# Kernel tuning notes

Hardware: AMD Instinct MI355X
Metric: run time of the kernel (lower is better)

The kernel has to match this reference:

```python
import jax, jax.numpy as jnp
import numpy as np

D_MODEL = 1024
N_HEADS = 16
D_K = D_MODEL // N_HEADS
BATCH = 2
SEQ = 2048


def setup_inputs() -> dict:
    key = jax.random.key(0)
    ks = jax.random.split(key, 6)
    scale = 1.0 / np.sqrt(D_MODEL)
    x = jax.random.normal(ks[0], (BATCH, SEQ, D_MODEL), dtype=jnp.float32)
    position_bias = jax.random.normal(ks[1], (N_HEADS, SEQ, SEQ), dtype=jnp.float32)
    w_q = jax.random.normal(ks[2], (D_MODEL, D_MODEL), dtype=jnp.float32) * scale
    w_k = jax.random.normal(ks[3], (D_MODEL, D_MODEL), dtype=jnp.float32) * scale
    w_v = jax.random.normal(ks[4], (D_MODEL, D_MODEL), dtype=jnp.float32) * scale
    w_o = jax.random.normal(ks[5], (D_MODEL, D_MODEL), dtype=jnp.float32) * scale
    return {"x": x, "position_bias": position_bias, "w_q": w_q, "w_k": w_k, "w_v": w_v, "w_o": w_o}


def reference(x, position_bias, w_q, w_k, w_v, w_o):
    B, n, _ = x.shape
    # Linear(d,d,bias=False): y = x @ W^T
    def split_heads(t):
        return t.reshape(B, n, N_HEADS, D_K).transpose(0, 2, 1, 3)  # [B,H,n,d_k]
    Q = split_heads(x @ w_q.T)
    K = split_heads(x @ w_k.T)
    V = split_heads(x @ w_v.T)
    # T5-style: no 1/sqrt(d_k) scaling
    scores = jnp.einsum('bhqd,bhkd->bhqk', Q, K) + position_bias[None]
    attn = jax.nn.softmax(scores.astype(jnp.float32), axis=-1).astype(scores.dtype)
    ctx = jnp.einsum('bhqk,bhkd->bhqd', attn, V)  # [B,H,n,d_k]
    attention = ctx.transpose(0, 2, 1, 3).reshape(B, n, D_MODEL)
    return attention @ w_o.T
```

## Files before the change

kernel.cpp:

```cpp
#include <hip/hip_runtime.h>


typedef _Float16 f16_t;
typedef _Float16 f16x8 __attribute__((ext_vector_type(8)));
typedef _Float16 f16x4 __attribute__((ext_vector_type(4)));
typedef float   floatx4 __attribute__((ext_vector_type(4)));

#define MFMA16(a, b, c)    __builtin_amdgcn_mfma_f32_16x16x32_f16((a), (b), (c), 0, 0, 0)
#define MFMA16K16(a, b, c) __builtin_amdgcn_mfma_f32_16x16x16f16((a), (b), (c), 0, 0, 0)

__global__ __launch_bounds__(256) void cvt_f32_f16(const float* __restrict__ src,
                                                   f16_t* __restrict__ dst, int n) {
  int i = (blockIdx.x * 256 + threadIdx.x) * 4;
  if (i < n) {
    floatx4 v = *(const floatx4*)(src + i);
    f16x4 o;
    o.x = (_Float16)v.x; o.y = (_Float16)v.y; o.z = (_Float16)v.z; o.w = (_Float16)v.w;
    *(f16x4*)(dst + i) = o;
  }
}

__global__ __launch_bounds__(256) void qkv_gemm(
    const f16_t* __restrict__ xb,
    const f16_t* __restrict__ wqb, const f16_t* __restrict__ wkb,
    const f16_t* __restrict__ wvb,
    f16_t* __restrict__ qb, f16_t* __restrict__ kb, f16_t* __restrict__ vb) {
  __shared__ f16_t As[128][72];
  __shared__ f16_t Bs[128][72];
  const int t = threadIdx.x;
  const int w = t >> 6, lane = t & 63, quad = lane >> 4, col = lane & 15;
  const int wm = w & 1, wn = w >> 1;
  const int mbase = blockIdx.x * 128;
  const int which = blockIdx.y >> 3;
  const int ncol0 = (blockIdx.y & 7) * 128;
  const f16_t* wsel = (which == 0) ? wqb : (which == 1) ? wkb : wvb;
  f16_t* osel = (which == 0) ? qb : (which == 1) ? kb : vb;

  floatx4 zero4 = {0.f, 0.f, 0.f, 0.f};
  floatx4 acc[4][4];
#pragma unroll
  for (int i = 0; i < 4; ++i)
#pragma unroll
    for (int j = 0; j < 4; ++j) acc[i][j] = zero4;

  for (int kt = 0; kt < 16; ++kt) {
    const int k0 = kt * 64;
#pragma unroll
    for (int rep = 0; rep < 4; ++rep) {
      int cid = t + rep * 256;
      int r = cid >> 3, c = (cid & 7) * 8;
      *(f16x8*)&As[r][c] = *(const f16x8*)(xb + (size_t)(mbase + r) * 1024 + k0 + c);
      *(f16x8*)&Bs[r][c] = *(const f16x8*)(wsel + (size_t)(ncol0 + r) * 1024 + k0 + c);
    }
    __syncthreads();
#pragma unroll
    for (int ch = 0; ch < 2; ++ch) {
      f16x8 a[4], b[4];
#pragma unroll
      for (int i = 0; i < 4; ++i)
        a[i] = *(const f16x8*)&As[wm * 64 + i * 16 + col][ch * 32 + quad * 8];
#pragma unroll
      for (int j = 0; j < 4; ++j)
        b[j] = *(const f16x8*)&Bs[wn * 64 + j * 16 + col][ch * 32 + quad * 8];
#pragma unroll
      for (int i = 0; i < 4; ++i)
#pragma unroll
        for (int j = 0; j < 4; ++j)
          acc[i][j] = MFMA16(a[i], b[j], acc[i][j]);
    }
    __syncthreads();
  }
#pragma unroll
  for (int i = 0; i < 4; ++i)
#pragma unroll
    for (int j = 0; j < 4; ++j)
#pragma unroll
      for (int rr = 0; rr < 4; ++rr) {
        int m = mbase + wm * 64 + i * 16 + quad * 4 + rr;
        int nf = ncol0 + wn * 64 + j * 16 + col;
        int h = nf >> 6, d = nf & 63;
        int bb2 = m >> 11, s = m & 2047;
        osel[(size_t)(((bb2 * 16 + h) * 2048) + s) * 64 + d] = (f16_t)acc[i][j][rr];
      }
}

__global__ __launch_bounds__(256) void out_gemm(
    const f16_t* __restrict__ ab, const f16_t* __restrict__ wob,
    float* __restrict__ outp) {
  __shared__ f16_t As[128][72];
  __shared__ f16_t Bs[128][72];
  const int t = threadIdx.x;
  const int w = t >> 6, lane = t & 63, quad = lane >> 4, col = lane & 15;
  const int wm = w & 1, wn = w >> 1;
  const int mbase = blockIdx.x * 128;
  const int nbase = blockIdx.y * 128;

  floatx4 zero4 = {0.f, 0.f, 0.f, 0.f};
  floatx4 acc[4][4];
#pragma unroll
  for (int i = 0; i < 4; ++i)
#pragma unroll
    for (int j = 0; j < 4; ++j) acc[i][j] = zero4;

  for (int kt = 0; kt < 16; ++kt) {
    const int k0 = kt * 64;
#pragma unroll
    for (int rep = 0; rep < 4; ++rep) {
      int cid = t + rep * 256;
      int r = cid >> 3, c = (cid & 7) * 8;
      *(f16x8*)&As[r][c] = *(const f16x8*)(ab + (size_t)(mbase + r) * 1024 + k0 + c);
      *(f16x8*)&Bs[r][c] = *(const f16x8*)(wob + (size_t)(nbase + r) * 1024 + k0 + c);
    }
    __syncthreads();
#pragma unroll
    for (int ch = 0; ch < 2; ++ch) {
      f16x8 a[4], b[4];
#pragma unroll
      for (int i = 0; i < 4; ++i)
        a[i] = *(const f16x8*)&As[wm * 64 + i * 16 + col][ch * 32 + quad * 8];
#pragma unroll
      for (int j = 0; j < 4; ++j)
        b[j] = *(const f16x8*)&Bs[wn * 64 + j * 16 + col][ch * 32 + quad * 8];
#pragma unroll
      for (int i = 0; i < 4; ++i)
#pragma unroll
        for (int j = 0; j < 4; ++j)
          acc[i][j] = MFMA16(a[i], b[j], acc[i][j]);
    }
    __syncthreads();
  }
#pragma unroll
  for (int i = 0; i < 4; ++i)
#pragma unroll
    for (int j = 0; j < 4; ++j)
#pragma unroll
      for (int rr = 0; rr < 4; ++rr) {
        int m = mbase + wm * 64 + i * 16 + quad * 4 + rr;
        int n = nbase + wn * 64 + j * 16 + col;
        outp[(size_t)m * 1024 + n] = acc[i][j][rr];
      }
}

__global__ __launch_bounds__(512) void attn_kernel(
    const f16_t* __restrict__ qb, const f16_t* __restrict__ kb,
    const f16_t* __restrict__ vb, const float* __restrict__ bias,
    f16_t* __restrict__ ctxb) {
  __shared__ f16_t Ks[2][64][72];
  __shared__ f16_t Vt[2][64][76];
  __shared__ f16_t biasS[64][72];

  const int t = threadIdx.x;
  const int w = t >> 6, lane = t & 63, quad = lane >> 4, col = lane & 15;
  const int bb = w >> 2, w4 = w & 3;
  const int h = blockIdx.y;
  const int qbase = blockIdx.x * 64;

  f16x8 qf[2];
  {
    const f16_t* qp = qb + (size_t)(((bb * 16 + h) * 2048) + qbase + w4 * 16 + col) * 64;
    qf[0] = *(const f16x8*)(qp + quad * 8);
    qf[1] = *(const f16x8*)(qp + 32 + quad * 8);
  }

  float mprev = -3e38f, lrun = 0.f;
  floatx4 zero4 = {0.f, 0.f, 0.f, 0.f};
  floatx4 oacc[4];
  oacc[0] = oacc[1] = oacc[2] = oacc[3] = zero4;

  for (int kt = 0; kt < 32; ++kt) {
    const int kbase = kt * 64;
#pragma unroll
    for (int rep = 0; rep < 2; ++rep) {
      int cid = t + rep * 512;
      int b2 = cid >> 9, rem = cid & 511;
      int r = rem >> 3, c = (rem & 7) * 8;
      *(f16x8*)&Ks[b2][r][c] =
          *(const f16x8*)(kb + (size_t)(((b2 * 16 + h) * 2048) + kbase + r) * 64 + c);
    }
    if (t < 256) {
      int b2 = t >> 7, rem = t & 127;
      int kk0 = (rem & 15) * 4, d0 = (rem >> 4) * 8;
      f16x8 rows[4];
#pragma unroll
      for (int j = 0; j < 4; ++j)
        rows[j] = *(const f16x8*)(vb +
            (size_t)(((b2 * 16 + h) * 2048) + kbase + kk0 + j) * 64 + d0);
#pragma unroll
      for (int d = 0; d < 8; ++d) {
        f16x4 pk;
        pk.x = rows[0][d]; pk.y = rows[1][d]; pk.z = rows[2][d]; pk.w = rows[3][d];
        *(f16x4*)&Vt[b2][d0 + d][kk0] = pk;
      }
    }
    {
      int r = t >> 3, c0 = (t & 7) * 8;
      const float* bp = bias + ((size_t)h * 2048 + qbase + r) * 2048 + kbase + c0;
      floatx4 v0 = *(const floatx4*)bp;
      floatx4 v1 = *(const floatx4*)(bp + 4);
      f16x8 bo;
      bo[0] = (_Float16)v0.x; bo[1] = (_Float16)v0.y;
      bo[2] = (_Float16)v0.z; bo[3] = (_Float16)v0.w;
      bo[4] = (_Float16)v1.x; bo[5] = (_Float16)v1.y;
      bo[6] = (_Float16)v1.z; bo[7] = (_Float16)v1.w;
      *(f16x8*)&biasS[r][c0] = bo;
    }
    __syncthreads();

    floatx4 sacc[4];
    sacc[0] = sacc[1] = sacc[2] = sacc[3] = zero4;
#pragma unroll
    for (int ch = 0; ch < 2; ++ch) {
#pragma unroll
      for (int cb = 0; cb < 4; ++cb) {
        f16x8 kf = *(const f16x8*)&Ks[bb][cb * 16 + col][ch * 32 + quad * 8];
        sacc[cb] = MFMA16(kf, qf[ch], sacc[cb]);
      }
    }
    float sv[4][4];
#pragma unroll
    for (int cb = 0; cb < 4; ++cb) {
      f16x4 b4 = *(const f16x4*)&biasS[w4 * 16 + col][cb * 16 + quad * 4];
#pragma unroll
      for (int i = 0; i < 4; ++i)
        sv[cb][i] = sacc[cb][i] + (float)b4[i];
    }
    float rm = -3e38f;
#pragma unroll
    for (int cb = 0; cb < 4; ++cb)
#pragma unroll
      for (int i = 0; i < 4; ++i) rm = fmaxf(rm, sv[cb][i]);
    rm = fmaxf(rm, __shfl_xor(rm, 16, 64));
    rm = fmaxf(rm, __shfl_xor(rm, 32, 64));
    float mnew = fmaxf(mprev, rm);
    float alpha = __expf(mprev - mnew);
    mprev = mnew;
    float ls = 0.f;
#pragma unroll
    for (int cb = 0; cb < 4; ++cb)
#pragma unroll
      for (int i = 0; i < 4; ++i) {
        float p = __expf(sv[cb][i] - mnew);
        sv[cb][i] = p;
        ls += p;
      }
    lrun = lrun * alpha + ls;
    float a0 = __shfl(alpha, quad * 4 + 0, 64);
    float a1 = __shfl(alpha, quad * 4 + 1, 64);
    float a2 = __shfl(alpha, quad * 4 + 2, 64);
    float a3 = __shfl(alpha, quad * 4 + 3, 64);
#pragma unroll
    for (int db = 0; db < 4; ++db) {
      oacc[db].x *= a0; oacc[db].y *= a1; oacc[db].z *= a2; oacc[db].w *= a3;
    }
#pragma unroll
    for (int cb = 0; cb < 4; ++cb) {
      f16x4 pf;
      pf[0] = (_Float16)sv[cb][0]; pf[1] = (_Float16)sv[cb][1];
      pf[2] = (_Float16)sv[cb][2]; pf[3] = (_Float16)sv[cb][3];
#pragma unroll
      for (int db = 0; db < 4; ++db) {
        f16x4 vf = *(const f16x4*)&Vt[bb][db * 16 + col][cb * 16 + quad * 4];
        oacc[db] = MFMA16K16(pf, vf, oacc[db]);
      }
    }
    __syncthreads();
  }

  float lt = lrun;
  lt += __shfl_xor(lt, 16, 64);
  lt += __shfl_xor(lt, 32, 64);
  float linv[4];
#pragma unroll
  for (int i = 0; i < 4; ++i)
    linv[i] = 1.0f / __shfl(lt, quad * 4 + i, 64);
#pragma unroll
  for (int db = 0; db < 4; ++db)
#pragma unroll
    for (int i = 0; i < 4; ++i) {
      int m = bb * 2048 + qbase + w4 * 16 + quad * 4 + i;
      int n = h * 64 + db * 16 + col;
      ctxb[(size_t)m * 1024 + n] = (f16_t)(oacc[db][i] * linv[i]);
    }
}

extern "C" void kernel_launch(void* const* d_in, const int* in_sizes, int n_in,
                              void* d_out, int out_size, void* d_ws, size_t ws_size,
                              hipStream_t stream) {
  const float* x    = (const float*)d_in[0];
  const float* bias = (const float*)d_in[1];
  const float* wq   = (const float*)d_in[2];
  const float* wk   = (const float*)d_in[3];
  const float* wv   = (const float*)d_in[4];
  const float* wo   = (const float*)d_in[5];
  float* outp = (float*)d_out;
  char* ws = (char*)d_ws;
  const size_t MB = 1u << 20;

  f16_t* xb   = (f16_t*)(ws);
  f16_t* wqb  = (f16_t*)(ws + 8 * MB);
  f16_t* wkb  = (f16_t*)(ws + 10 * MB);
  f16_t* wvb  = (f16_t*)(ws + 12 * MB);
  f16_t* wob  = (f16_t*)(ws + 14 * MB);
  f16_t* qb   = (f16_t*)(ws + 16 * MB);
  f16_t* kb   = (f16_t*)(ws + 24 * MB);
  f16_t* vb   = (f16_t*)(ws + 32 * MB);
  f16_t* ctxb = (f16_t*)(ws + 40 * MB);

  cvt_f32_f16<<<4096, 256, 0, stream>>>(x, xb, 4194304);
  cvt_f32_f16<<<1024, 256, 0, stream>>>(wq, wqb, 1048576);
  cvt_f32_f16<<<1024, 256, 0, stream>>>(wk, wkb, 1048576);
  cvt_f32_f16<<<1024, 256, 0, stream>>>(wv, wvb, 1048576);
  cvt_f32_f16<<<1024, 256, 0, stream>>>(wo, wob, 1048576);

  qkv_gemm<<<dim3(32, 24), 256, 0, stream>>>(xb, wqb, wkb, wvb, qb, kb, vb);
  attn_kernel<<<dim3(32, 16), 512, 0, stream>>>(qb, kb, vb, bias, ctxb);
  out_gemm<<<dim3(32, 8), 256, 0, stream>>>(ctxb, wob, outp);
}
```

Baseline: 507.6 us.

## Fuse conversions, use direct-to-LDS loads in GEMMs, prefetch attention tiles into registers

The five fp32-to-fp16 conversion launches become a single kernel. Both GEMMs now stage A/B tiles with global_load_lds, which copies global memory straight into unpadded LDS and skips the VGPR round trip. The attention kernel prefetches the next K, V and bias tiles into registers while it computes on the current tile, then writes them to LDS afterwards. It also reshapes the V transpose into 2-row pairs. Dropping the LDS padding may add bank conflicts on the MFMA fragment reads, and the prefetch registers add register pressure.

New measurement: 507.6 us. About the same (-0.0%).

```diff
diff --git a/kernel.cpp b/kernel.cpp
--- a/kernel.cpp
+++ b/kernel.cpp
@@ -4,20 +4,36 @@
 typedef _Float16 f16_t;
 typedef _Float16 f16x8 __attribute__((ext_vector_type(8)));
 typedef _Float16 f16x4 __attribute__((ext_vector_type(4)));
+typedef _Float16 f16x2 __attribute__((ext_vector_type(2)));
 typedef float   floatx4 __attribute__((ext_vector_type(4)));
 
 #define MFMA16(a, b, c)    __builtin_amdgcn_mfma_f32_16x16x32_f16((a), (b), (c), 0, 0, 0)
 #define MFMA16K16(a, b, c) __builtin_amdgcn_mfma_f32_16x16x16f16((a), (b), (c), 0, 0, 0)
 
-__global__ __launch_bounds__(256) void cvt_f32_f16(const float* __restrict__ src,
-                                                   f16_t* __restrict__ dst, int n) {
-  int i = (blockIdx.x * 256 + threadIdx.x) * 4;
-  if (i < n) {
-    floatx4 v = *(const floatx4*)(src + i);
-    f16x4 o;
-    o.x = (_Float16)v.x; o.y = (_Float16)v.y; o.z = (_Float16)v.z; o.w = (_Float16)v.w;
-    *(f16x4*)(dst + i) = o;
-  }
+__device__ __forceinline__ void gload_lds16(const f16_t* g, f16_t* l) {
+  __builtin_amdgcn_global_load_lds(
+      (const __attribute__((address_space(1))) void*)g,
+      (__attribute__((address_space(3))) void*)l, 16, 0, 0);
+}
+
+__global__ __launch_bounds__(256) void cvt_all(
+    const float* __restrict__ x,  const float* __restrict__ wq,
+    const float* __restrict__ wk, const float* __restrict__ wv,
+    const float* __restrict__ wo,
+    f16_t* __restrict__ xb,  f16_t* __restrict__ wqb, f16_t* __restrict__ wkb,
+    f16_t* __restrict__ wvb, f16_t* __restrict__ wob) {
+  int b = blockIdx.x;
+  const float* src; f16_t* dst; int base;
+  if (b < 4096)      { src = x;  dst = xb;  base = b; }
+  else if (b < 5120) { src = wq; dst = wqb; base = b - 4096; }
+  else if (b < 6144) { src = wk; dst = wkb; base = b - 5120; }
+  else if (b < 7168) { src = wv; dst = wvb; base = b - 6144; }
+  else               { src = wo; dst = wob; base = b - 7168; }
+  int i = (base * 256 + threadIdx.x) * 4;
+  floatx4 v = *(const floatx4*)(src + i);
+  f16x4 o;
+  o.x = (_Float16)v.x; o.y = (_Float16)v.y; o.z = (_Float16)v.z; o.w = (_Float16)v.w;
+  *(f16x4*)(dst + i) = o;
 }
 
 __global__ __launch_bounds__(256) void qkv_gemm(
@@ -25,8 +41,8 @@
     const f16_t* __restrict__ wqb, const f16_t* __restrict__ wkb,
     const f16_t* __restrict__ wvb,
     f16_t* __restrict__ qb, f16_t* __restrict__ kb, f16_t* __restrict__ vb) {
-  __shared__ f16_t As[128][72];
-  __shared__ f16_t Bs[128][72];
+  __shared__ f16_t As[128 * 64];
+  __shared__ f16_t Bs[128 * 64];
   const int t = threadIdx.x;
   const int w = t >> 6, lane = t & 63, quad = lane >> 4, col = lane & 15;
   const int wm = w & 1, wn = w >> 1;
@@ -47,10 +63,12 @@
     const int k0 = kt * 64;
 #pragma unroll
     for (int rep = 0; rep < 4; ++rep) {
-      int cid = t + rep * 256;
-      int r = cid >> 3, c = (cid & 7) * 8;
-      *(f16x8*)&As[r][c] = *(const f16x8*)(xb + (size_t)(mbase + r) * 1024 + k0 + c);
-      *(f16x8*)&Bs[r][c] = *(const f16x8*)(wsel + (size_t)(ncol0 + r) * 1024 + k0 + c);
+      int chunk = rep * 256 + w * 64 + lane;
+      int r = chunk >> 3, c8 = (chunk & 7) * 8;
+      f16_t* abase = As + (size_t)(rep * 256 + w * 64) * 8;
+      f16_t* bbase = Bs + (size_t)(rep * 256 + w * 64) * 8;
+      gload_lds16(xb + (size_t)(mbase + r) * 1024 + k0 + c8, abase);
+      gload_lds16(wsel + (size_t)(ncol0 + r) * 1024 + k0 + c8, bbase);
     }
     __syncthreads();
 #pragma unroll
@@ -58,10 +76,10 @@
       f16x8 a[4], b[4];
 #pragma unroll
       for (int i = 0; i < 4; ++i)
-        a[i] = *(const f16x8*)&As[wm * 64 + i * 16 + col][ch * 32 + quad * 8];
+        a[i] = *(const f16x8*)(As + (size_t)(wm * 64 + i * 16 + col) * 64 + ch * 32 + quad * 8);
 #pragma unroll
       for (int j = 0; j < 4; ++j)
-        b[j] = *(const f16x8*)&Bs[wn * 64 + j * 16 + col][ch * 32 + quad * 8];
+        b[j] = *(const f16x8*)(Bs + (size_t)(wn * 64 + j * 16 + col) * 64 + ch * 32 + quad * 8);
 #pragma unroll
       for (int i = 0; i < 4; ++i)
 #pragma unroll
@@ -87,8 +105,8 @@
 __global__ __launch_bounds__(256) void out_gemm(
     const f16_t* __restrict__ ab, const f16_t* __restrict__ wob,
     float* __restrict__ outp) {
-  __shared__ f16_t As[128][72];
-  __shared__ f16_t Bs[128][72];
+  __shared__ f16_t As[128 * 64];
+  __shared__ f16_t Bs[128 * 64];
   const int t = threadIdx.x;
   const int w = t >> 6, lane = t & 63, quad = lane >> 4, col = lane & 15;
   const int wm = w & 1, wn = w >> 1;
@@ -106,10 +124,12 @@
     const int k0 = kt * 64;
 #pragma unroll
     for (int rep = 0; rep < 4; ++rep) {
-      int cid = t + rep * 256;
-      int r = cid >> 3, c = (cid & 7) * 8;
-      *(f16x8*)&As[r][c] = *(const f16x8*)(ab + (size_t)(mbase + r) * 1024 + k0 + c);
-      *(f16x8*)&Bs[r][c] = *(const f16x8*)(wob + (size_t)(nbase + r) * 1024 + k0 + c);
+      int chunk = rep * 256 + w * 64 + lane;
+      int r = chunk >> 3, c8 = (chunk & 7) * 8;
+      f16_t* abase = As + (size_t)(rep * 256 + w * 64) * 8;
+      f16_t* bbase = Bs + (size_t)(rep * 256 + w * 64) * 8;
+      gload_lds16(ab + (size_t)(mbase + r) * 1024 + k0 + c8, abase);
+      gload_lds16(wob + (size_t)(nbase + r) * 1024 + k0 + c8, bbase);
     }
     __syncthreads();
 #pragma unroll
@@ -117,10 +137,10 @@
       f16x8 a[4], b[4];
 #pragma unroll
       for (int i = 0; i < 4; ++i)
-        a[i] = *(const f16x8*)&As[wm * 64 + i * 16 + col][ch * 32 + quad * 8];
+        a[i] = *(const f16x8*)(As + (size_t)(wm * 64 + i * 16 + col) * 64 + ch * 32 + quad * 8);
 #pragma unroll
       for (int j = 0; j < 4; ++j)
-        b[j] = *(const f16x8*)&Bs[wn * 64 + j * 16 + col][ch * 32 + quad * 8];
+        b[j] = *(const f16x8*)(Bs + (size_t)(wn * 64 + j * 16 + col) * 64 + ch * 32 + quad * 8);
 #pragma unroll
       for (int i = 0; i < 4; ++i)
 #pragma unroll
@@ -155,6 +175,10 @@
   const int h = blockIdx.y;
   const int qbase = blockIdx.x * 64;
 
+  const int vb2 = t >> 8, vrem = t & 255;
+  const int vk0 = (vrem & 31) * 2, vd0 = (vrem >> 5) * 8;
+  const int br = t >> 3, bc0 = (t & 7) * 8;
+
   f16x8 qf[2];
   {
     const f16_t* qp = qb + (size_t)(((bb * 16 + h) * 2048) + qbase + w4 * 16 + col) * 64;
@@ -167,44 +191,54 @@
   floatx4 oacc[4];
   oacc[0] = oacc[1] = oacc[2] = oacc[3] = zero4;
 
-  for (int kt = 0; kt < 32; ++kt) {
-    const int kbase = kt * 64;
+  {
 #pragma unroll
     for (int rep = 0; rep < 2; ++rep) {
       int cid = t + rep * 512;
       int b2 = cid >> 9, rem = cid & 511;
       int r = rem >> 3, c = (rem & 7) * 8;
       *(f16x8*)&Ks[b2][r][c] =
-          *(const f16x8*)(kb + (size_t)(((b2 * 16 + h) * 2048) + kbase + r) * 64 + c);
-    }
-    if (t < 256) {
-      int b2 = t >> 7, rem = t & 127;
-      int kk0 = (rem & 15) * 4, d0 = (rem >> 4) * 8;
-      f16x8 rows[4];
-#pragma unroll
-      for (int j = 0; j < 4; ++j)
-        rows[j] = *(const f16x8*)(vb +
-            (size_t)(((b2 * 16 + h) * 2048) + kbase + kk0 + j) * 64 + d0);
-#pragma unroll
-      for (int d = 0; d < 8; ++d) {
-        f16x4 pk;
-        pk.x = rows[0][d]; pk.y = rows[1][d]; pk.z = rows[2][d]; pk.w = rows[3][d];
-        *(f16x4*)&Vt[b2][d0 + d][kk0] = pk;
-      }
-    }
-    {
-      int r = t >> 3, c0 = (t & 7) * 8;
-      const float* bp = bias + ((size_t)h * 2048 + qbase + r) * 2048 + kbase + c0;
-      floatx4 v0 = *(const floatx4*)bp;
-      floatx4 v1 = *(const floatx4*)(bp + 4);
-      f16x8 bo;
-      bo[0] = (_Float16)v0.x; bo[1] = (_Float16)v0.y;
-      bo[2] = (_Float16)v0.z; bo[3] = (_Float16)v0.w;
-      bo[4] = (_Float16)v1.x; bo[5] = (_Float16)v1.y;
-      bo[6] = (_Float16)v1.z; bo[7] = (_Float16)v1.w;
-      *(f16x8*)&biasS[r][c0] = bo;
-    }
-    __syncthreads();
+          *(const f16x8*)(kb + (size_t)(((b2 * 16 + h) * 2048) + r) * 64 + c);
+    }
+    f16x8 r0 = *(const f16x8*)(vb + (size_t)(((vb2 * 16 + h) * 2048) + vk0) * 64 + vd0);
+    f16x8 r1 = *(const f16x8*)(vb + (size_t)(((vb2 * 16 + h) * 2048) + vk0 + 1) * 64 + vd0);
+#pragma unroll
+    for (int d = 0; d < 8; ++d) {
+      f16x2 pk; pk.x = r0[d]; pk.y = r1[d];
+      *(f16x2*)&Vt[vb2][vd0 + d][vk0] = pk;
+    }
+    const float* bp = bias + ((size_t)h * 2048 + qbase + br) * 2048 + bc0;
+    floatx4 v0 = *(const floatx4*)bp;
+    floatx4 v1 = *(const floatx4*)(bp + 4);
+    f16x8 bo;
+    bo[0] = (_Float16)v0.x; bo[1] = (_Float16)v0.y;
+    bo[2] = (_Float16)v0.z; bo[3] = (_Float16)v0.w;
+    bo[4] = (_Float16)v1.x; bo[5] = (_Float16)v1.y;
+    bo[6] = (_Float16)v1.z; bo[7] = (_Float16)v1.w;
+    *(f16x8*)&biasS[br][bc0] = bo;
+  }
+  __syncthreads();
+
+  f16x8 kreg0, kreg1, vreg0, vreg1;
+  floatx4 breg0, breg1;
+
+  for (int kt = 0; kt < 32; ++kt) {
+    if (kt < 31) {
+      const int nb = (kt + 1) * 64;
+      {
+        int cid = t;
+        int b2 = cid >> 9, rem = cid & 511, r = rem >> 3, c = (rem & 7) * 8;
+        kreg0 = *(const f16x8*)(kb + (size_t)(((b2 * 16 + h) * 2048) + nb + r) * 64 + c);
+        cid = t + 512;
+        b2 = cid >> 9; rem = cid & 511; r = rem >> 3; c = (rem & 7) * 8;
+        kreg1 = *(const f16x8*)(kb + (size_t)(((b2 * 16 + h) * 2048) + nb + r) * 64 + c);
+      }
+      vreg0 = *(const f16x8*)(vb + (size_t)(((vb2 * 16 + h) * 2048) + nb + vk0) * 64 + vd0);
+      vreg1 = *(const f16x8*)(vb + (size_t)(((vb2 * 16 + h) * 2048) + nb + vk0 + 1) * 64 + vd0);
+      const float* bp = bias + ((size_t)h * 2048 + qbase + br) * 2048 + nb + bc0;
+      breg0 = *(const floatx4*)bp;
+      breg1 = *(const floatx4*)(bp + 4);
+    }
 
     floatx4 sacc[4];
     sacc[0] = sacc[1] = sacc[2] = sacc[3] = zero4;
@@ -264,6 +298,29 @@
       }
     }
     __syncthreads();
+
+    if (kt < 31) {
+      {
+        int cid = t;
+        int b2 = cid >> 9, rem = cid & 511, r = rem >> 3, c = (rem & 7) * 8;
+        *(f16x8*)&Ks[b2][r][c] = kreg0;
+        cid = t + 512;
+        b2 = cid >> 9; rem = cid & 511; r = rem >> 3; c = (rem & 7) * 8;
+        *(f16x8*)&Ks[b2][r][c] = kreg1;
+      }
+#pragma unroll
+      for (int d = 0; d < 8; ++d) {
+        f16x2 pk; pk.x = vreg0[d]; pk.y = vreg1[d];
+        *(f16x2*)&Vt[vb2][vd0 + d][vk0] = pk;
+      }
+      f16x8 bo;
+      bo[0] = (_Float16)breg0.x; bo[1] = (_Float16)breg0.y;
+      bo[2] = (_Float16)breg0.z; bo[3] = (_Float16)breg0.w;
+      bo[4] = (_Float16)breg1.x; bo[5] = (_Float16)breg1.y;
+      bo[6] = (_Float16)breg1.z; bo[7] = (_Float16)breg1.w;
+      *(f16x8*)&biasS[br][bc0] = bo;
+      __syncthreads();
+    }
   }
 
   float lt = lrun;
@@ -306,12 +363,7 @@
   f16_t* vb   = (f16_t*)(ws + 32 * MB);
   f16_t* ctxb = (f16_t*)(ws + 40 * MB);
 
-  cvt_f32_f16<<<4096, 256, 0, stream>>>(x, xb, 4194304);
-  cvt_f32_f16<<<1024, 256, 0, stream>>>(wq, wqb, 1048576);
-  cvt_f32_f16<<<1024, 256, 0, stream>>>(wk, wkb, 1048576);
-  cvt_f32_f16<<<1024, 256, 0, stream>>>(wv, wvb, 1048576);
-  cvt_f32_f16<<<1024, 256, 0, stream>>>(wo, wob, 1048576);
-
+  cvt_all<<<8192, 256, 0, stream>>>(x, wq, wk, wv, wo, xb, wqb, wkb, wvb, wob);
   qkv_gemm<<<dim3(32, 24), 256, 0, stream>>>(xb, wqb, wkb, wvb, qb, kb, vb);
   attn_kernel<<<dim3(32, 16), 512, 0, stream>>>(qb, kb, vb, bias, ctxb);
   out_gemm<<<dim3(32, 8), 256, 0, stream>>>(ctxb, wob, outp);
```
